# Performance work log

Measured on AMD Instinct MI355X. Metric: run time of the kernel, lower is better.

Reference implementation:

```python
import jax, jax.numpy as jnp
import numpy as np

FEATS = 1024
HEAD = 16
MLP_HIDDEN = 4096
B, N = 8, 1024
EPS = 1e-5


def _layernorm(x, g, b):
    mu = jnp.mean(x, axis=-1, keepdims=True)
    var = jnp.var(x, axis=-1, keepdims=True)
    return (x - mu) * jax.lax.rsqrt(var + EPS) * g + b


def setup_inputs() -> dict:
    key = jax.random.key(0)
    ks = jax.random.split(key, 12)
    s_attn = 1.0 / np.sqrt(FEATS)
    s_mlp1 = 1.0 / np.sqrt(FEATS)
    s_mlp2 = 1.0 / np.sqrt(MLP_HIDDEN)
    return {
        "x": jax.random.normal(ks[0], (B, N, FEATS), dtype=jnp.float32),
        "ln1_g": jnp.ones((FEATS,), jnp.float32),
        "ln1_b": jnp.zeros((FEATS,), jnp.float32),
        "wq": jax.random.normal(ks[1], (FEATS, FEATS), jnp.float32) * s_attn,
        "bq": jnp.zeros((FEATS,), jnp.float32),
        "wk": jax.random.normal(ks[2], (FEATS, FEATS), jnp.float32) * s_attn,
        "bk": jnp.zeros((FEATS,), jnp.float32),
        "wv": jax.random.normal(ks[3], (FEATS, FEATS), jnp.float32) * s_attn,
        "bv": jnp.zeros((FEATS,), jnp.float32),
        "wo": jax.random.normal(ks[4], (FEATS, FEATS), jnp.float32) * s_attn,
        "bo": jnp.zeros((FEATS,), jnp.float32),
        "ln2_g": jnp.ones((FEATS,), jnp.float32),
        "ln2_b": jnp.zeros((FEATS,), jnp.float32),
        "w1": jax.random.normal(ks[5], (FEATS, MLP_HIDDEN), jnp.float32) * s_mlp1,
        "b1": jnp.zeros((MLP_HIDDEN,), jnp.float32),
        "w2": jax.random.normal(ks[6], (MLP_HIDDEN, FEATS), jnp.float32) * s_mlp2,
        "b2": jnp.zeros((FEATS,), jnp.float32),
    }


def reference(x, ln1_g, ln1_b, wq, bq, wk, bk, wv, bv, wo, bo,
              ln2_g, ln2_b, w1, b1, w2, b2):
    b, n, f = x.shape
    d = f // HEAD
    sqrt_d = jnp.asarray(f, x.dtype) ** 0.5  # NOTE: scale by sqrt(feats), as in source

    h = _layernorm(x, ln1_g, ln1_b)
    # [b, n, f] -> [b, head, n, d]
    q = (h @ wq + bq).reshape(b, n, HEAD, d).transpose(0, 2, 1, 3)
    k = (h @ wk + bk).reshape(b, n, HEAD, d).transpose(0, 2, 1, 3)
    v = (h @ wv + bv).reshape(b, n, HEAD, d).transpose(0, 2, 1, 3)

    score = jnp.einsum('bhif,bhjf->bhij', q, k) / sqrt_d
    p = jax.nn.softmax(score, axis=-1)
    attn = jnp.einsum('bhij,bhjf->bihf', p, v).reshape(b, n, f)
    o = attn @ wo + bo
    out = o + x

    h2 = _layernorm(out, ln2_g, ln2_b)
    m = jax.nn.gelu(h2 @ w1 + b1, approximate=False)
    m = jax.nn.gelu(m @ w2 + b2, approximate=False)
    return m + out
```

## Files before the change

kernel.cpp:

```cpp
#include <hip/hip_runtime.h>
#include <cstdint>

typedef __bf16 bf16;
typedef __attribute__((ext_vector_type(8))) __bf16 bf16x8;
typedef __attribute__((ext_vector_type(4))) __bf16 bf16x4;
typedef __attribute__((ext_vector_type(4))) float f32x4;
typedef __attribute__((ext_vector_type(8))) unsigned short u16x8;

#define AS1C(p) ((const __attribute__((address_space(1))) void*)(p))
#define AS3(p)  ((__attribute__((address_space(3))) void*)(p))

__device__ __forceinline__ float gelu_exact(float v) {
    return 0.5f * v * (1.0f + erff(v * 0.7071067811865476f));
}

__global__ __launch_bounds__(256, 1) void wtrans_kernel(
    const float* __restrict__ w, bf16* __restrict__ wt, int K, int N)
{
    __shared__ float tile[64][65];
    const int k0 = blockIdx.y * 64, n0 = blockIdx.x * 64;
    const int tid = threadIdx.x;
    {
        const int kl = tid >> 2, nc = (tid & 3) * 16;
        #pragma unroll
        for (int i = 0; i < 4; ++i) {
            const float4 v = *(const float4*)&w[(size_t)(k0 + kl) * N + n0 + nc + i * 4];
            tile[kl][nc + i * 4 + 0] = v.x;
            tile[kl][nc + i * 4 + 1] = v.y;
            tile[kl][nc + i * 4 + 2] = v.z;
            tile[kl][nc + i * 4 + 3] = v.w;
        }
    }
    __syncthreads();
    {
        const int nl = tid >> 2, kc = (tid & 3) * 16;
        #pragma unroll
        for (int i = 0; i < 4; ++i) {
            bf16x4 o4;
            o4[0] = (bf16)tile[kc + i * 4 + 0][nl];
            o4[1] = (bf16)tile[kc + i * 4 + 1][nl];
            o4[2] = (bf16)tile[kc + i * 4 + 2][nl];
            o4[3] = (bf16)tile[kc + i * 4 + 3][nl];
            *(bf16x4*)&wt[(size_t)(n0 + nl) * K + k0 + kc + i * 4] = o4;
        }
    }
}

__global__ void bias3_kernel(const float* __restrict__ a, const float* __restrict__ b,
                             const float* __restrict__ c, float* __restrict__ o)
{
    const int i = blockIdx.x * 256 + threadIdx.x;
    o[i] = (i < 1024) ? a[i] : (i < 2048 ? b[i - 1024] : c[i - 2048]);
}

__global__ __launch_bounds__(256, 1) void ln_kernel(
    const float* __restrict__ x, const float* __restrict__ gw,
    const float* __restrict__ bw, bf16* __restrict__ out)
{
    const int row = blockIdx.x, tid = threadIdx.x;
    const float4 v = *(const float4*)&x[(size_t)row * 1024 + tid * 4];
    float s = v.x + v.y + v.z + v.w;
    float q = v.x * v.x + v.y * v.y + v.z * v.z + v.w * v.w;
    #pragma unroll
    for (int off = 32; off > 0; off >>= 1) {
        s += __shfl_xor(s, off);
        q += __shfl_xor(q, off);
    }
    __shared__ float red[8];
    if ((tid & 63) == 0) { red[tid >> 6] = s; red[4 + (tid >> 6)] = q; }
    __syncthreads();
    s = red[0] + red[1] + red[2] + red[3];
    q = red[4] + red[5] + red[6] + red[7];
    const float mu = s * (1.f / 1024.f);
    const float rs = rsqrtf(q * (1.f / 1024.f) - mu * mu + 1e-5f);
    const float4 gg = *(const float4*)&gw[tid * 4];
    const float4 bb = *(const float4*)&bw[tid * 4];
    bf16x4 o4;
    o4[0] = (bf16)((v.x - mu) * rs * gg.x + bb.x);
    o4[1] = (bf16)((v.y - mu) * rs * gg.y + bb.y);
    o4[2] = (bf16)((v.z - mu) * rs * gg.z + bb.z);
    o4[3] = (bf16)((v.w - mu) * rs * gg.w + bb.w);
    *(bf16x4*)&out[(size_t)row * 1024 + tid * 4] = o4;
}

template<int EPI, int BM>
__global__ __launch_bounds__(256, 2) void gemm_v6_kernel(
    const bf16* __restrict__ A, const bf16* __restrict__ BT,
    const float* __restrict__ bias, const float* __restrict__ res,
    void* __restrict__ out, int M, int N, int K)
{
    constexpr int BN = 384 - BM;
    constexpr int ABYTES = BM * 64;
    constexpr int BUFB = 384 * 64;
    extern __shared__ char lds[];

    const int tid = threadIdx.x;
    const int lane = tid & 63, wid = tid >> 6;
    const int wr = (BM == 256) ? (wid >> 1) : 0;
    const int wc = (BM == 256) ? (wid & 1) : wid;
    const int j = lane & 15, g = lane >> 4;
    const int srow = tid >> 2;
    const int skc = ((tid & 3) ^ ((tid >> 3) & 3)) << 3;

    const int nbn = N / BN;
    const int nwg = (M / BM) * nbn;
    const int bid = blockIdx.x;
    const int wg = (bid & 7) * (nwg >> 3) + (bid >> 3);
    const int bm = (wg / nbn) * BM;
    const int bn = (wg % nbn) * BN;

    auto stage = [&](int k0, char* obuf) {
        #pragma unroll
        for (int ga = 0; ga < BM / 64; ++ga) {
            const bf16* src = A + (size_t)(bm + ga * 64 + srow) * K + k0 + skc;
            __builtin_amdgcn_global_load_lds(AS1C(src), AS3(obuf + ga * 4096 + tid * 16), 16, 0, 0);
        }
        #pragma unroll
        for (int gb = 0; gb < BN / 64; ++gb) {
            const bf16* src = BT + (size_t)(bn + gb * 64 + srow) * K + k0 + skc;
            __builtin_amdgcn_global_load_lds(AS1C(src), AS3(obuf + ABYTES + gb * 4096 + tid * 16), 16, 0, 0);
        }
    };

    f32x4 acc[8][4] = {};
    const int NT = K >> 5;

    stage(0, lds);
    stage(32, lds + BUFB);
    asm volatile("s_waitcnt vmcnt(6)" ::: "memory");
    __builtin_amdgcn_s_barrier();

    int cur = 0;
    for (int t = 0; t < NT; ++t) {
        char* buf = lds + cur * BUFB;
        const int nxt2 = (cur + 2 >= 3) ? cur - 1 : cur + 2;

        bf16x8 af[8], bfr[2];
        #pragma unroll
        for (int mf = 0; mf < 8; ++mf) {
            const int R = wr * 128 + mf * 16 + j;
            uint32_t lb = (uint32_t)(R * 64 + g * 16);
            lb ^= ((lb >> 7) & 3u) << 4;
            af[mf] = *(const bf16x8*)(buf + lb);
        }
        #pragma unroll
        for (int nf = 0; nf < 2; ++nf) {
            const int R = wc * 64 + nf * 16 + j;
            uint32_t lb = (uint32_t)(R * 64 + g * 16);
            lb ^= ((lb >> 7) & 3u) << 4;
            bfr[nf] = *(const bf16x8*)(buf + ABYTES + lb);
        }
        if (t + 2 < NT) stage((t + 2) << 5, lds + nxt2 * BUFB);
        __builtin_amdgcn_s_barrier();
        asm volatile("s_waitcnt lgkmcnt(0)" ::: "memory");
        __builtin_amdgcn_sched_barrier(0);
        __builtin_amdgcn_s_setprio(1);
        #pragma unroll
        for (int mf = 0; mf < 8; ++mf)
            #pragma unroll
            for (int nf = 0; nf < 2; ++nf)
                acc[mf][nf] = __builtin_amdgcn_mfma_f32_16x16x32_bf16(
                    af[mf], bfr[nf], acc[mf][nf], 0, 0, 0);
        __builtin_amdgcn_s_setprio(0);
        __builtin_amdgcn_s_barrier();

        bf16x8 bfr2[2];
        #pragma unroll
        for (int nf = 0; nf < 2; ++nf) {
            const int R = wc * 64 + (2 + nf) * 16 + j;
            uint32_t lb = (uint32_t)(R * 64 + g * 16);
            lb ^= ((lb >> 7) & 3u) << 4;
            bfr2[nf] = *(const bf16x8*)(buf + ABYTES + lb);
        }
        __builtin_amdgcn_s_barrier();
        asm volatile("s_waitcnt lgkmcnt(0)" ::: "memory");
        __builtin_amdgcn_sched_barrier(0);
        __builtin_amdgcn_s_setprio(1);
        #pragma unroll
        for (int mf = 0; mf < 8; ++mf)
            #pragma unroll
            for (int nf = 0; nf < 2; ++nf)
                acc[mf][2 + nf] = __builtin_amdgcn_mfma_f32_16x16x32_bf16(
                    af[mf], bfr2[nf], acc[mf][2 + nf], 0, 0, 0);
        __builtin_amdgcn_s_setprio(0);
        if (t + 2 < NT) asm volatile("s_waitcnt vmcnt(6)" ::: "memory");
        else            asm volatile("s_waitcnt vmcnt(0)" ::: "memory");
        __builtin_amdgcn_s_barrier();

        cur = (cur + 1 >= 3) ? 0 : cur + 1;
    }

    const int row0 = bm + wr * 128;
    const int col0 = bn + wc * 64;
    #pragma unroll
    for (int nf = 0; nf < 4; ++nf) {
        const int col = col0 + nf * 16 + j;
        const float bs = bias[col];
        #pragma unroll
        for (int mf = 0; mf < 8; ++mf) {
            #pragma unroll
            for (int r = 0; r < 4; ++r) {
                const int row = row0 + mf * 16 + g * 4 + r;
                float v = acc[mf][nf][r] + bs;
                if constexpr (EPI == 2 || EPI == 3) v = gelu_exact(v);
                if constexpr (EPI == 1 || EPI == 3) {
                    v += res[(size_t)row * N + col];
                    ((float*)out)[(size_t)row * N + col] = v;
                } else {
                    ((bf16*)out)[(size_t)row * N + col] = (bf16)v;
                }
            }
        }
    }
}

__device__ __forceinline__ void attn_iter(
    int c, const bf16* __restrict__ Kp, const bf16* __restrict__ Vp,
    uint32_t (&vTu)[3][64][36],
    bf16x8 (&kf)[4][2], bf16x8 (&kfn)[4][2],
    const bf16x8& qf0, const bf16x8& qf1,
    f32x4 (&o)[4], float& mrun, float& lsum,
    int kp, int d0, int jperm, int g, int j)
{
    const f32x4 zero = {0.f, 0.f, 0.f, 0.f};
    const bool pfv = (c + 2 < 16);
    const bool pfk = (c + 1 < 16);

    u16x8 r0, r1;
    if (pfv) {
        const size_t vb = (size_t)((c + 2) * 64 + kp) * 3072 + d0;
        r0 = *(const u16x8*)&Vp[vb];
        r1 = *(const u16x8*)&Vp[vb + 3072];
    }

    f32x4 s[4];
    #pragma unroll
    for (int t = 0; t < 4; ++t) {
        s[t] = __builtin_amdgcn_mfma_f32_16x16x32_bf16(kf[t][0], qf0, zero, 0, 0, 0);
        s[t] = __builtin_amdgcn_mfma_f32_16x16x32_bf16(kf[t][1], qf1, s[t], 0, 0, 0);
    }

    if (pfk) {
        #pragma unroll
        for (int t = 0; t < 4; ++t) {
            const int key = (c + 1) * 64 + (t >> 1) * 32 + jperm + (t & 1) * 4;
            kfn[t][0] = *(const bf16x8*)&Kp[(size_t)key * 3072 + g * 8];
            kfn[t][1] = *(const bf16x8*)&Kp[(size_t)key * 3072 + 32 + g * 8];
        }
    }

    float cur = fmaxf(fmaxf(s[0][0], s[0][1]), fmaxf(s[0][2], s[0][3]));
    #pragma unroll
    for (int t = 1; t < 4; ++t)
        cur = fmaxf(cur, fmaxf(fmaxf(s[t][0], s[t][1]), fmaxf(s[t][2], s[t][3])));
    cur = fmaxf(cur, __shfl_xor(cur, 16));
    cur = fmaxf(cur, __shfl_xor(cur, 32));

    if (!__all(cur - mrun <= 8.0f)) {
        const float mnew = fmaxf(mrun, cur);
        const float alpha = __expf(mrun - mnew);
        float al[4];
        #pragma unroll
        for (int r = 0; r < 4; ++r) al[r] = __shfl(alpha, g * 4 + r);
        #pragma unroll
        for (int dt = 0; dt < 4; ++dt)
            #pragma unroll
            for (int r = 0; r < 4; ++r) o[dt][r] *= al[r];
        lsum *= alpha;
        mrun = mnew;
    }
    float ps = 0.f;
    #pragma unroll
    for (int t = 0; t < 4; ++t)
        #pragma unroll
        for (int r = 0; r < 4; ++r) {
            const float p = __expf(s[t][r] - mrun);
            s[t][r] = p;
            ps += p;
        }
    lsum += ps;

    bf16x8 pa0, pa1;
    #pragma unroll
    for (int r = 0; r < 4; ++r) {
        pa0[r]     = (bf16)s[0][r];
        pa0[4 + r] = (bf16)s[1][r];
        pa1[r]     = (bf16)s[2][r];
        pa1[4 + r] = (bf16)s[3][r];
    }

    if (pfv) {
        const int wb = (c + 2) % 3;
        #pragma unroll
        for (int i = 0; i < 8; ++i)
            vTu[wb][d0 + i][kp >> 1] = (uint32_t)r0[i] | ((uint32_t)r1[i] << 16);
    }

    const int rb = c % 3;
    #pragma unroll
    for (int dt = 0; dt < 4; ++dt) {
        const bf16* vrow = (const bf16*)&vTu[rb][dt * 16 + j][0];
        const bf16x8 vb0 = *(const bf16x8*)(vrow + g * 8);
        const bf16x8 vb1 = *(const bf16x8*)(vrow + 32 + g * 8);
        o[dt] = __builtin_amdgcn_mfma_f32_16x16x32_bf16(pa0, vb0, o[dt], 0, 0, 0);
        o[dt] = __builtin_amdgcn_mfma_f32_16x16x32_bf16(pa1, vb1, o[dt], 0, 0, 0);
    }
}

__global__ __launch_bounds__(256, 1) void attn_kernel(
    const bf16* __restrict__ qkv, bf16* __restrict__ attn, int bh_base)
{
    const int tid = threadIdx.x;
    const int lane = tid & 63, wid = tid >> 6;
    const int j = lane & 15, g = lane >> 4;

    const int lin = blockIdx.x + blockIdx.y * 16;
    const int virt = (lin & 7) * 128 + (lin >> 3);
    const int bh = bh_base + (virt >> 4), qt = virt & 15;
    const int b = bh >> 4, h = bh & 15;
    const int q0 = qt * 64 + wid * 16;

    const bf16* Qp = qkv + (size_t)b * 1024 * 3072 + h * 64;
    const bf16* Kp = Qp + 1024;
    const bf16* Vp = Qp + 2048;

    __shared__ __attribute__((aligned(16))) uint32_t vTu[3][64][36];

    const int kp = (tid & 31) * 2;
    const int d0 = (tid >> 5) * 8;
    #pragma unroll
    for (int pb = 0; pb < 2; ++pb) {
        const u16x8 r0 = *(const u16x8*)&Vp[(size_t)(pb * 64 + kp) * 3072 + d0];
        const u16x8 r1 = *(const u16x8*)&Vp[(size_t)(pb * 64 + kp + 1) * 3072 + d0];
        #pragma unroll
        for (int i = 0; i < 8; ++i)
            vTu[pb][d0 + i][kp >> 1] = (uint32_t)r0[i] | ((uint32_t)r1[i] << 16);
    }

    bf16x8 qf0 = *(const bf16x8*)&Qp[(size_t)(q0 + j) * 3072 + g * 8];
    bf16x8 qf1 = *(const bf16x8*)&Qp[(size_t)(q0 + j) * 3072 + 32 + g * 8];
    #pragma unroll
    for (int e = 0; e < 8; ++e) {
        qf0[e] = (bf16)((float)qf0[e] * 0.03125f);
        qf1[e] = (bf16)((float)qf1[e] * 0.03125f);
    }

    const int jperm = (j >> 2) * 8 + (j & 3);

    f32x4 o[4] = {};
    float mrun = -1e30f, lsum = 0.f;

    bf16x8 kfA[4][2], kfB[4][2];
    #pragma unroll
    for (int t = 0; t < 4; ++t) {
        const int key = (t >> 1) * 32 + jperm + (t & 1) * 4;
        kfA[t][0] = *(const bf16x8*)&Kp[(size_t)key * 3072 + g * 8];
        kfA[t][1] = *(const bf16x8*)&Kp[(size_t)key * 3072 + 32 + g * 8];
    }

    asm volatile("s_waitcnt lgkmcnt(0)" ::: "memory");
    __builtin_amdgcn_s_barrier();

    for (int cc = 0; cc < 16; cc += 2) {
        attn_iter(cc,     Kp, Vp, vTu, kfA, kfB, qf0, qf1, o, mrun, lsum, kp, d0, jperm, g, j);
        attn_iter(cc + 1, Kp, Vp, vTu, kfB, kfA, qf0, qf1, o, mrun, lsum, kp, d0, jperm, g, j);
        asm volatile("s_waitcnt lgkmcnt(0)" ::: "memory");
        __builtin_amdgcn_sched_barrier(0);
        __builtin_amdgcn_s_barrier();
    }

    lsum += __shfl_xor(lsum, 16);
    lsum += __shfl_xor(lsum, 32);
    float inv[4];
    #pragma unroll
    for (int r = 0; r < 4; ++r) inv[r] = 1.0f / __shfl(lsum, g * 4 + r);
    #pragma unroll
    for (int dt = 0; dt < 4; ++dt)
        #pragma unroll
        for (int r = 0; r < 4; ++r)
            attn[(size_t)(b * 1024 + q0 + g * 4 + r) * 1024 + h * 64 + dt * 16 + j] =
                (bf16)(o[dt][r] * inv[r]);
}

extern "C" void kernel_launch(void* const* d_in, const int* in_sizes, int n_in,
                              void* d_out, int out_size, void* d_ws, size_t ws_size,
                              hipStream_t stream)
{
    const float* x    = (const float*)d_in[0];
    const float* ln1g = (const float*)d_in[1];
    const float* ln1b = (const float*)d_in[2];
    const float* wq   = (const float*)d_in[3];
    const float* bq   = (const float*)d_in[4];
    const float* wk   = (const float*)d_in[5];
    const float* bk   = (const float*)d_in[6];
    const float* wv   = (const float*)d_in[7];
    const float* bv   = (const float*)d_in[8];
    const float* wo   = (const float*)d_in[9];
    const float* bo   = (const float*)d_in[10];
    const float* ln2g = (const float*)d_in[11];
    const float* ln2b = (const float*)d_in[12];
    const float* w1   = (const float*)d_in[13];
    const float* b1   = (const float*)d_in[14];
    const float* w2   = (const float*)d_in[15];
    const float* b2   = (const float*)d_in[16];

    char* ws = (char*)d_ws;
    bf16* wqkvT = (bf16*)ws;  ws += (size_t)3072 * 1024 * 2;
    bf16* woT   = (bf16*)ws;  ws += (size_t)1024 * 1024 * 2;
    bf16* w1T   = (bf16*)ws;  ws += (size_t)4096 * 1024 * 2;
    bf16* w2T   = (bf16*)ws;  ws += (size_t)1024 * 4096 * 2;
    float* bqkv = (float*)ws; ws += (size_t)3072 * 4;
    bf16* h     = (bf16*)ws;  ws += (size_t)8192 * 1024 * 2;
    bf16* qkv   = (bf16*)ws;  ws += (size_t)8192 * 3072 * 2;
    bf16* attn  = (bf16*)ws;  ws += (size_t)8192 * 1024 * 2;
    float* outf = (float*)ws; ws += (size_t)8192 * 1024 * 4;
    bf16* m1    = (bf16*)ws;  ws += (size_t)8192 * 4096 * 2;

    (void)hipFuncSetAttribute((const void*)gemm_v6_kernel<0, 128>,
                              hipFuncAttributeMaxDynamicSharedMemorySize, 73728);
    (void)hipFuncSetAttribute((const void*)gemm_v6_kernel<1, 256>,
                              hipFuncAttributeMaxDynamicSharedMemorySize, 73728);
    (void)hipFuncSetAttribute((const void*)gemm_v6_kernel<2, 128>,
                              hipFuncAttributeMaxDynamicSharedMemorySize, 73728);
    (void)hipFuncSetAttribute((const void*)gemm_v6_kernel<3, 256>,
                              hipFuncAttributeMaxDynamicSharedMemorySize, 73728);

    wtrans_kernel<<<dim3(16, 16), 256, 0, stream>>>(wq, wqkvT,                   1024, 1024);
    wtrans_kernel<<<dim3(16, 16), 256, 0, stream>>>(wk, wqkvT + 1024 * 1024,     1024, 1024);
    wtrans_kernel<<<dim3(16, 16), 256, 0, stream>>>(wv, wqkvT + 2 * 1024 * 1024, 1024, 1024);
    wtrans_kernel<<<dim3(16, 16), 256, 0, stream>>>(wo, woT, 1024, 1024);
    wtrans_kernel<<<dim3(64, 16), 256, 0, stream>>>(w1, w1T, 1024, 4096);
    wtrans_kernel<<<dim3(16, 64), 256, 0, stream>>>(w2, w2T, 4096, 1024);
    bias3_kernel<<<12, 256, 0, stream>>>(bq, bk, bv, bqkv);

    ln_kernel<<<8192, 256, 0, stream>>>(x, ln1g, ln1b, h);
    gemm_v6_kernel<0, 128><<<768, 256, 73728, stream>>>(h, wqkvT, bqkv, nullptr, qkv, 8192, 3072, 1024);
    attn_kernel<<<dim3(16, 64), 256, 0, stream>>>(qkv, attn, 0);
    attn_kernel<<<dim3(16, 64), 256, 0, stream>>>(qkv, attn, 64);
    gemm_v6_kernel<1, 256><<<256, 256, 73728, stream>>>(attn, woT, bo, x, outf, 8192, 1024, 1024);
    ln_kernel<<<8192, 256, 0, stream>>>(outf, ln2g, ln2b, h);
    gemm_v6_kernel<2, 128><<<1024, 256, 73728, stream>>>(h, w1T, b1, nullptr, m1, 8192, 4096, 1024);
    gemm_v6_kernel<3, 256><<<256, 256, 73728, stream>>>(m1, w2T, b2, outf, (float*)d_out, 8192, 1024, 4096);
}
```

Before: 551.7 us.

## Restructure GEMM to 512-thread 256x128 tiles with 64-deep K steps

The templated GEMM with configurable BM and a 32-wide K step is replaced by a single 8-wave kernel. It uses a 256x128 output tile, a 64-wide K step with a wider XOR swizzle, and triple-buffered LDS at 144KB per block. The goal is to halve the number of K-loop iterations and barriers per tile and to give every GEMM the same tile shape. The large LDS footprint likely limits each CU to one workgroup, which gives up the two-block overlap the old launch bounds allowed. Separately, the attention V-transpose ring buffer grows from 3 to 4 slots so the modulo becomes a bitmask.

```diff
diff --git a/kernel.cpp b/kernel.cpp
--- a/kernel.cpp
+++ b/kernel.cpp
@@ -83,121 +83,128 @@
     *(bf16x4*)&out[(size_t)row * 1024 + tid * 4] = o4;
 }
 
-template<int EPI, int BM>
-__global__ __launch_bounds__(256, 2) void gemm_v6_kernel(
+template<int EPI>
+__global__ __launch_bounds__(512, 2) void gemm_v7_kernel(
     const bf16* __restrict__ A, const bf16* __restrict__ BT,
     const float* __restrict__ bias, const float* __restrict__ res,
     void* __restrict__ out, int M, int N, int K)
 {
-    constexpr int BN = 384 - BM;
-    constexpr int ABYTES = BM * 64;
-    constexpr int BUFB = 384 * 64;
+    constexpr int ABYTES = 256 * 128;
+    constexpr int BUFB = 384 * 128;
     extern __shared__ char lds[];
 
     const int tid = threadIdx.x;
     const int lane = tid & 63, wid = tid >> 6;
-    const int wr = (BM == 256) ? (wid >> 1) : 0;
-    const int wc = (BM == 256) ? (wid & 1) : wid;
+    const int wr = wid >> 1, wc = wid & 1;
     const int j = lane & 15, g = lane >> 4;
-    const int srow = tid >> 2;
-    const int skc = ((tid & 3) ^ ((tid >> 3) & 3)) << 3;
-
-    const int nbn = N / BN;
-    const int nwg = (M / BM) * nbn;
+    const int skc = ((tid & 7) ^ ((tid >> 4) & 7)) << 3;
+
+    const int nbn = N >> 7;
+    const int nwg = (M >> 8) * nbn;
     const int bid = blockIdx.x;
     const int wg = (bid & 7) * (nwg >> 3) + (bid >> 3);
-    const int bm = (wg / nbn) * BM;
-    const int bn = (wg % nbn) * BN;
+    const int bm = (wg / nbn) << 8;
+    const int bn = (wg % nbn) << 7;
 
     auto stage = [&](int k0, char* obuf) {
         #pragma unroll
-        for (int ga = 0; ga < BM / 64; ++ga) {
-            const bf16* src = A + (size_t)(bm + ga * 64 + srow) * K + k0 + skc;
-            __builtin_amdgcn_global_load_lds(AS1C(src), AS3(obuf + ga * 4096 + tid * 16), 16, 0, 0);
-        }
-        #pragma unroll
-        for (int gb = 0; gb < BN / 64; ++gb) {
-            const bf16* src = BT + (size_t)(bn + gb * 64 + srow) * K + k0 + skc;
-            __builtin_amdgcn_global_load_lds(AS1C(src), AS3(obuf + ABYTES + gb * 4096 + tid * 16), 16, 0, 0);
+        for (int ga = 0; ga < 4; ++ga) {
+            const bf16* src = A + (size_t)(bm + ga * 64 + (tid >> 3)) * K + k0 + skc;
+            __builtin_amdgcn_global_load_lds(AS1C(src), AS3(obuf + ga * 8192 + tid * 16), 16, 0, 0);
+        }
+        #pragma unroll
+        for (int gb = 0; gb < 2; ++gb) {
+            const bf16* src = BT + (size_t)(bn + gb * 64 + (tid >> 3)) * K + k0 + skc;
+            __builtin_amdgcn_global_load_lds(AS1C(src), AS3(obuf + ABYTES + gb * 8192 + tid * 16), 16, 0, 0);
         }
     };
 
-    f32x4 acc[8][4] = {};
-    const int NT = K >> 5;
+    f32x4 acc[4][4] = {};
+    const int NT = K >> 6;
 
     stage(0, lds);
-    stage(32, lds + BUFB);
+    stage(64, lds + BUFB);
     asm volatile("s_waitcnt vmcnt(6)" ::: "memory");
     __builtin_amdgcn_s_barrier();
 
     int cur = 0;
     for (int t = 0; t < NT; ++t) {
         char* buf = lds + cur * BUFB;
-        const int nxt2 = (cur + 2 >= 3) ? cur - 1 : cur + 2;
-
-        bf16x8 af[8], bfr[2];
-        #pragma unroll
-        for (int mf = 0; mf < 8; ++mf) {
-            const int R = wr * 128 + mf * 16 + j;
-            uint32_t lb = (uint32_t)(R * 64 + g * 16);
-            lb ^= ((lb >> 7) & 3u) << 4;
-            af[mf] = *(const bf16x8*)(buf + lb);
-        }
-        #pragma unroll
-        for (int nf = 0; nf < 2; ++nf) {
-            const int R = wc * 64 + nf * 16 + j;
-            uint32_t lb = (uint32_t)(R * 64 + g * 16);
-            lb ^= ((lb >> 7) & 3u) << 4;
-            bfr[nf] = *(const bf16x8*)(buf + ABYTES + lb);
-        }
-        if (t + 2 < NT) stage((t + 2) << 5, lds + nxt2 * BUFB);
+        const int nxt2 = (cur >= 1) ? cur - 1 : 2;
+
+        bf16x8 af[4][2], bfr[2][2];
+        #pragma unroll
+        for (int mf = 0; mf < 4; ++mf)
+            #pragma unroll
+            for (int ks = 0; ks < 2; ++ks) {
+                const int R = wr * 64 + mf * 16 + j;
+                uint32_t lb = (uint32_t)(R * 128 + ks * 64 + g * 16);
+                lb ^= (lb >> 4) & 0x70u;
+                af[mf][ks] = *(const bf16x8*)(buf + lb);
+            }
+        #pragma unroll
+        for (int nf = 0; nf < 2; ++nf)
+            #pragma unroll
+            for (int ks = 0; ks < 2; ++ks) {
+                const int R = wc * 64 + nf * 16 + j;
+                uint32_t lb = (uint32_t)(R * 128 + ks * 64 + g * 16);
+                lb ^= (lb >> 4) & 0x70u;
+                bfr[nf][ks] = *(const bf16x8*)(buf + ABYTES + lb);
+            }
+        if (t + 2 < NT) stage((t + 2) << 6, lds + nxt2 * BUFB);
         __builtin_amdgcn_s_barrier();
         asm volatile("s_waitcnt lgkmcnt(0)" ::: "memory");
         __builtin_amdgcn_sched_barrier(0);
         __builtin_amdgcn_s_setprio(1);
         #pragma unroll
-        for (int mf = 0; mf < 8; ++mf)
+        for (int mf = 0; mf < 4; ++mf)
             #pragma unroll
             for (int nf = 0; nf < 2; ++nf)
-                acc[mf][nf] = __builtin_amdgcn_mfma_f32_16x16x32_bf16(
-                    af[mf], bfr[nf], acc[mf][nf], 0, 0, 0);
+                #pragma unroll
+                for (int ks = 0; ks < 2; ++ks)
+                    acc[mf][nf] = __builtin_amdgcn_mfma_f32_16x16x32_bf16(
+                        af[mf][ks], bfr[nf][ks], acc[mf][nf], 0, 0, 0);
         __builtin_amdgcn_s_setprio(0);
         __builtin_amdgcn_s_barrier();
 
-        bf16x8 bfr2[2];
-        #pragma unroll
-        for (int nf = 0; nf < 2; ++nf) {
-            const int R = wc * 64 + (2 + nf) * 16 + j;
-            uint32_t lb = (uint32_t)(R * 64 + g * 16);
-            lb ^= ((lb >> 7) & 3u) << 4;
-            bfr2[nf] = *(const bf16x8*)(buf + ABYTES + lb);
-        }
+        bf16x8 bfr2[2][2];
+        #pragma unroll
+        for (int nf = 0; nf < 2; ++nf)
+            #pragma unroll
+            for (int ks = 0; ks < 2; ++ks) {
+                const int R = wc * 64 + (2 + nf) * 16 + j;
+                uint32_t lb = (uint32_t)(R * 128 + ks * 64 + g * 16);
+                lb ^= (lb >> 4) & 0x70u;
+                bfr2[nf][ks] = *(const bf16x8*)(buf + ABYTES + lb);
+            }
         __builtin_amdgcn_s_barrier();
         asm volatile("s_waitcnt lgkmcnt(0)" ::: "memory");
         __builtin_amdgcn_sched_barrier(0);
         __builtin_amdgcn_s_setprio(1);
         #pragma unroll
-        for (int mf = 0; mf < 8; ++mf)
+        for (int mf = 0; mf < 4; ++mf)
             #pragma unroll
             for (int nf = 0; nf < 2; ++nf)
-                acc[mf][2 + nf] = __builtin_amdgcn_mfma_f32_16x16x32_bf16(
-                    af[mf], bfr2[nf], acc[mf][2 + nf], 0, 0, 0);
+                #pragma unroll
+                for (int ks = 0; ks < 2; ++ks)
+                    acc[mf][2 + nf] = __builtin_amdgcn_mfma_f32_16x16x32_bf16(
+                        af[mf][ks], bfr2[nf][ks], acc[mf][2 + nf], 0, 0, 0);
         __builtin_amdgcn_s_setprio(0);
         if (t + 2 < NT) asm volatile("s_waitcnt vmcnt(6)" ::: "memory");
         else            asm volatile("s_waitcnt vmcnt(0)" ::: "memory");
         __builtin_amdgcn_s_barrier();
 
-        cur = (cur + 1 >= 3) ? 0 : cur + 1;
-    }
-
-    const int row0 = bm + wr * 128;
+        cur = (cur == 2) ? 0 : cur + 1;
+    }
+
+    const int row0 = bm + wr * 64;
     const int col0 = bn + wc * 64;
     #pragma unroll
     for (int nf = 0; nf < 4; ++nf) {
         const int col = col0 + nf * 16 + j;
         const float bs = bias[col];
         #pragma unroll
-        for (int mf = 0; mf < 8; ++mf) {
+        for (int mf = 0; mf < 4; ++mf) {
             #pragma unroll
             for (int r = 0; r < 4; ++r) {
                 const int row = row0 + mf * 16 + g * 4 + r;
@@ -216,7 +223,7 @@
 
 __device__ __forceinline__ void attn_iter(
     int c, const bf16* __restrict__ Kp, const bf16* __restrict__ Vp,
-    uint32_t (&vTu)[3][64][36],
+    uint32_t (&vTu)[4][64][36],
     bf16x8 (&kf)[4][2], bf16x8 (&kfn)[4][2],
     const bf16x8& qf0, const bf16x8& qf1,
     f32x4 (&o)[4], float& mrun, float& lsum,
@@ -290,13 +297,13 @@
     }
 
     if (pfv) {
-        const int wb = (c + 2) % 3;
+        const int wb = (c + 2) & 3;
         #pragma unroll
         for (int i = 0; i < 8; ++i)
             vTu[wb][d0 + i][kp >> 1] = (uint32_t)r0[i] | ((uint32_t)r1[i] << 16);
     }
 
-    const int rb = c % 3;
+    const int rb = c & 3;
     #pragma unroll
     for (int dt = 0; dt < 4; ++dt) {
         const bf16* vrow = (const bf16*)&vTu[rb][dt * 16 + j][0];
@@ -324,7 +331,7 @@
     const bf16* Kp = Qp + 1024;
     const bf16* Vp = Qp + 2048;
 
-    __shared__ __attribute__((aligned(16))) uint32_t vTu[3][64][36];
+    __shared__ __attribute__((aligned(16))) uint32_t vTu[4][64][36];
 
     const int kp = (tid & 31) * 2;
     const int d0 = (tid >> 5) * 8;
@@ -416,14 +423,14 @@
     float* outf = (float*)ws; ws += (size_t)8192 * 1024 * 4;
     bf16* m1    = (bf16*)ws;  ws += (size_t)8192 * 4096 * 2;
 
-    (void)hipFuncSetAttribute((const void*)gemm_v6_kernel<0, 128>,
-                              hipFuncAttributeMaxDynamicSharedMemorySize, 73728);
-    (void)hipFuncSetAttribute((const void*)gemm_v6_kernel<1, 256>,
-                              hipFuncAttributeMaxDynamicSharedMemorySize, 73728);
-    (void)hipFuncSetAttribute((const void*)gemm_v6_kernel<2, 128>,
-                              hipFuncAttributeMaxDynamicSharedMemorySize, 73728);
-    (void)hipFuncSetAttribute((const void*)gemm_v6_kernel<3, 256>,
-                              hipFuncAttributeMaxDynamicSharedMemorySize, 73728);
+    (void)hipFuncSetAttribute((const void*)gemm_v7_kernel<0>,
+                              hipFuncAttributeMaxDynamicSharedMemorySize, 147456);
+    (void)hipFuncSetAttribute((const void*)gemm_v7_kernel<1>,
+                              hipFuncAttributeMaxDynamicSharedMemorySize, 147456);
+    (void)hipFuncSetAttribute((const void*)gemm_v7_kernel<2>,
+                              hipFuncAttributeMaxDynamicSharedMemorySize, 147456);
+    (void)hipFuncSetAttribute((const void*)gemm_v7_kernel<3>,
+                              hipFuncAttributeMaxDynamicSharedMemorySize, 147456);
 
     wtrans_kernel<<<dim3(16, 16), 256, 0, stream>>>(wq, wqkvT,                   1024, 1024);
     wtrans_kernel<<<dim3(16, 16), 256, 0, stream>>>(wk, wqkvT + 1024 * 1024,     1024, 1024);
@@ -434,11 +441,11 @@
     bias3_kernel<<<12, 256, 0, stream>>>(bq, bk, bv, bqkv);
 
     ln_kernel<<<8192, 256, 0, stream>>>(x, ln1g, ln1b, h);
-    gemm_v6_kernel<0, 128><<<768, 256, 73728, stream>>>(h, wqkvT, bqkv, nullptr, qkv, 8192, 3072, 1024);
+    gemm_v7_kernel<0><<<768, 512, 147456, stream>>>(h, wqkvT, bqkv, nullptr, qkv, 8192, 3072, 1024);
     attn_kernel<<<dim3(16, 64), 256, 0, stream>>>(qkv, attn, 0);
     attn_kernel<<<dim3(16, 64), 256, 0, stream>>>(qkv, attn, 64);
-    gemm_v6_kernel<1, 256><<<256, 256, 73728, stream>>>(attn, woT, bo, x, outf, 8192, 1024, 1024);
+    gemm_v7_kernel<1><<<256, 512, 147456, stream>>>(attn, woT, bo, x, outf, 8192, 1024, 1024);
     ln_kernel<<<8192, 256, 0, stream>>>(outf, ln2g, ln2b, h);
-    gemm_v6_kernel<2, 128><<<1024, 256, 73728, stream>>>(h, w1T, b1, nullptr, m1, 8192, 4096, 1024);
-    gemm_v6_kernel<3, 256><<<256, 256, 73728, stream>>>(m1, w2T, b2, outf, (float*)d_out, 8192, 1024, 4096);
-}
+    gemm_v7_kernel<2><<<1024, 512, 147456, stream>>>(h, w1T, b1, nullptr, m1, 8192, 4096, 1024);
+    gemm_v7_kernel<3><<<256, 512, 147456, stream>>>(m1, w2T, b2, outf, (float*)d_out, 8192, 1024, 4096);
+}
```

Result: faster. 511.9 us (-7.2%).
